# Kernel tuning notes

Hardware: AMD Instinct MI355X
Metric: run time of the kernel (lower is better)

## Reference

```python
import jax, jax.numpy as jnp
import numpy as np

ALPHA = 0.0005
TAU = 0.2


def setup_inputs() -> dict:
    key = jax.random.key(0)
    k1, k2, k3 = jax.random.split(key, 3)
    x_batch = jax.random.normal(k1, (2048, 4096), dtype=jnp.float32)
    y_batch = jax.random.normal(k2, (2048, 4096), dtype=jnp.float32)
    # conv weight [out_ch, in_ch, kh, kw]; sliced along dim 2 (F = 64)
    conv_w = jax.random.normal(k3, (512, 512, 64, 3), dtype=jnp.float32) * 0.05
    return {"x_batch": x_batch, "y_batch": y_batch, "conv_w": conv_w}


def _diversity_reg(conv_w, tau):
    # slices conv_w[:, :, i, :] flattened -> rows of v: [F, out*in*kw]
    F = conv_w.shape[2]
    v = jnp.transpose(conv_w, (2, 0, 1, 3)).reshape(F, -1)
    norms = jnp.sqrt(jnp.sum(v * v, axis=1))  # [F]
    gram = v @ v.T  # [F, F] -- memory-bound tall-skinny reduction
    sim = gram / (norms[:, None] * norms[None, :])
    eye = jnp.eye(F, dtype=bool)
    # keep iff tau < sim <= 1 and i != j; zeroed entries are detached (constant 0)
    mask = (sim > tau) & (sim <= 1.0) & (~eye)
    return jnp.sum(jnp.where(mask, sim, 0.0))


def reference(x_batch, y_batch, conv_w):
    # loss_function = MSELoss (mean reduction)
    loss_value = jnp.mean((x_batch - y_batch) ** 2)
    reg_value = _diversity_reg(conv_w, TAU)
    return loss_value + ALPHA * reg_value
```

## Files before the change

kernel.cpp:

```cpp
#include <hip/hip_runtime.h>

typedef __attribute__((ext_vector_type(8)))  short   short8;
typedef __attribute__((ext_vector_type(4)))  unsigned uint4v;
typedef __attribute__((ext_vector_type(16))) float   f32x16;
typedef __attribute__((ext_vector_type(4)))  float   f4;

constexpr int GRAM_BLOCKS = 384;
constexpr int MSE_BLOCKS  = 128;
constexpr int BLOCK       = 256;
constexpr int CHUNK_F     = 3072;
constexpr int NCHUNK      = 16384;
constexpr int GRAM_WAVES  = GRAM_BLOCKS * 4;
constexpr int MSE_THREADS = MSE_BLOCKS * BLOCK;
constexpr int RED_BLOCKS  = 96;

constexpr int MSE_OFF  = 0;
constexpr int FLAG_OFF = 128;
constexpr int GF_OFF   = 256;
constexpr int PART_OFF = 4096;

struct F3 { float v[3]; };
struct Chunk { F3 a0[4], a1[4], b0[4], b1[4]; };

__device__ __forceinline__ unsigned pk_bf16(float a, float b) {
  unsigned a2 = __builtin_bit_cast(unsigned, a) + 0x8000u;
  unsigned b2 = __builtin_bit_cast(unsigned, b) + 0x8000u;
  return __builtin_amdgcn_perm(b2, a2, 0x07060302u);
}

__device__ __forceinline__ void load_chunk(const float* __restrict__ W, int c,
                                           int laneoff, Chunk& ch) {
  const float* s = W + (size_t)c * CHUNK_F + laneoff;
#pragma unroll
  for (int bp = 0; bp < 4; ++bp) {
    const float* p = s + bp * 384;
    ch.a0[bp] = *(const F3*)(p);
    ch.a1[bp] = *(const F3*)(p + 96);
    ch.b0[bp] = *(const F3*)(p + 192);
    ch.b1[bp] = *(const F3*)(p + 288);
  }
}

__device__ __forceinline__ void mac_chunk(const Chunk& c, f32x16& a00, f32x16& a01,
                                          f32x16& a11) {
#pragma unroll
  for (int k = 0; k < 3; ++k) {
    unsigned fl[4], fh[4];
#pragma unroll
    for (int bp = 0; bp < 4; ++bp) {
      fl[bp] = pk_bf16(c.a0[bp].v[k], c.b0[bp].v[k]);
      fh[bp] = pk_bf16(c.a1[bp].v[k], c.b1[bp].v[k]);
    }
    uint4v vl = {fl[0], fl[1], fl[2], fl[3]};
    uint4v vh = {fh[0], fh[1], fh[2], fh[3]};
    short8 lo = __builtin_bit_cast(short8, vl);
    short8 hv = __builtin_bit_cast(short8, vh);
    a00 = __builtin_amdgcn_mfma_f32_32x32x16_bf16(lo, lo, a00, 0, 0, 0);
    a01 = __builtin_amdgcn_mfma_f32_32x32x16_bf16(lo, hv, a01, 0, 0, 0);
    a11 = __builtin_amdgcn_mfma_f32_32x32x16_bf16(hv, hv, a11, 0, 0, 0);
  }
}

__global__ __launch_bounds__(BLOCK, 2) void k_a(
    const float* __restrict__ X, const float* __restrict__ Y,
    const float* __restrict__ W, float* __restrict__ ws) {
  __shared__ __align__(16) float red[2][3072];
  const int bid = blockIdx.x;
  const int tid = threadIdx.x;
  const int wave = tid >> 6;
  const int lane = tid & 63;

  if (bid >= GRAM_BLOCKS) {
    const unsigned t0 = (unsigned)((bid - GRAM_BLOCKS) * BLOCK + tid);
    const f4* x4 = (const f4*)X;
    const f4* y4 = (const f4*)Y;
    float acc = 0.f;
#pragma unroll 8
    for (int it = 0; it < 64; ++it) {
      unsigned i = t0 + (unsigned)it * (unsigned)MSE_THREADS;
      f4 a = __builtin_nontemporal_load(x4 + i);
      f4 b = __builtin_nontemporal_load(y4 + i);
      float d0 = a[0] - b[0], d1 = a[1] - b[1], d2 = a[2] - b[2], d3 = a[3] - b[3];
      acc += d0 * d0 + d1 * d1 + d2 * d2 + d3 * d3;
    }
#pragma unroll
    for (int o = 32; o; o >>= 1) acc += __shfl_xor(acc, o, 64);
    __shared__ float wsum[4];
    if (lane == 0) wsum[wave] = acc;
    __syncthreads();
    if (tid == 0) ws[MSE_OFF + bid - GRAM_BLOCKS] = wsum[0] + wsum[1] + wsum[2] + wsum[3];
    return;
  }

  const int r    = lane & 31;
  const int hi   = lane >> 5;
  const int laneoff = hi * 1536 + 3 * r;
  const int wg = bid * 4 + wave;

  f32x16 a00{}, a01{}, a11{};
  Chunk ca, cb;
  int c = wg;
  load_chunk(W, c, laneoff, ca);
  c += GRAM_WAVES;
  for (;;) {
    if (c < NCHUNK) load_chunk(W, c, laneoff, cb);
    mac_chunk(ca, a00, a01, a11);
    if (c >= NCHUNK) break;
    c += GRAM_WAVES;
    if (c < NCHUNK) load_chunk(W, c, laneoff, ca);
    mac_chunk(cb, a00, a01, a11);
    if (c >= NCHUNK) break;
    c += GRAM_WAVES;
  }

  if (wave < 2) {
#pragma unroll
    for (int rg = 0; rg < 16; ++rg) {
      red[wave][       rg * 64 + lane] = a00[rg];
      red[wave][1024 + rg * 64 + lane] = a01[rg];
      red[wave][2048 + rg * 64 + lane] = a11[rg];
    }
  }
  __syncthreads();
  if (wave >= 2) {
    float* dst = red[wave - 2];
#pragma unroll
    for (int rg = 0; rg < 16; ++rg) {
      dst[       rg * 64 + lane] += a00[rg];
      dst[1024 + rg * 64 + lane] += a01[rg];
      dst[2048 + rg * 64 + lane] += a11[rg];
    }
  }
  __syncthreads();
  const f4* r0 = (const f4*)&red[0][0];
  const f4* r1 = (const f4*)&red[1][0];
  f4* p4 = (f4*)(ws + PART_OFF + (size_t)bid * 3072);
#pragma unroll
  for (int q = tid; q < 768; q += BLOCK) {
    f4 a = r0[q], b = r1[q];
    p4[q] = a + b;
  }
}

__global__ __launch_bounds__(256) void k_b(float* __restrict__ ws,
                                           float* __restrict__ out) {
  __shared__ float r2[4][32];
  __shared__ float g[3072];
  __shared__ float n2[64];
  __shared__ float msum_s[4];
  __shared__ float wsum[4];
  const int tid = threadIdx.x;
  const int lane = tid & 63, wv = tid >> 6, el = lane & 31, ph = lane >> 5;
  const int b = blockIdx.x;
  const int w0 = b * 32;
  int* flags = (int*)(ws + FLAG_OFF);

  const float* base = ws + PART_OFF + (size_t)(ph + 2 * wv) * 3072 + w0 + el;
  float acc = 0.f;
#pragma unroll 8
  for (int i = 0; i < 48; ++i) acc += base[(size_t)i * 24576];
  acc += __shfl_xor(acc, 32, 64);
  if (ph == 0) r2[wv][el] = acc;
  __syncthreads();
  if (tid < 32)
    ws[GF_OFF + w0 + tid] = r2[0][tid] + r2[1][tid] + r2[2][tid] + r2[3][tid];
  __syncthreads();
  if (tid == 0) {
    __threadfence();
    __hip_atomic_store(&flags[b], 1, __ATOMIC_RELEASE, __HIP_MEMORY_SCOPE_AGENT);
  }
  if (b != 0) return;

  if (tid < RED_BLOCKS) {
    while (__hip_atomic_load(&flags[tid], __ATOMIC_RELAXED,
                             __HIP_MEMORY_SCOPE_AGENT) != 1)
      __builtin_amdgcn_s_sleep(8);
  }
  __syncthreads();
  __threadfence();

  for (int e = tid; e < 3072; e += 256) g[e] = ws[GF_OFF + e];

  float m = (tid < 128) ? ws[MSE_OFF + tid] : 0.f;
#pragma unroll
  for (int o = 32; o; o >>= 1) m += __shfl_xor(m, o, 64);
  if (lane == 0) msum_s[wv] = m;
  __syncthreads();

  if (tid < RED_BLOCKS) flags[tid] = 0;

  for (int e = tid; e < 3072; e += 256) {
    int tl = e >> 10, rg = (e >> 6) & 15, l = e & 63;
    int il = (rg & 3) + 8 * (rg >> 2) + 4 * (l >> 5);
    int jl = l & 31;
    if (tl != 1 && il == jl) n2[il + (tl == 2 ? 32 : 0)] = g[e];
  }
  __syncthreads();

  float local = 0.f;
  for (int e = tid; e < 3072; e += 256) {
    int tl = e >> 10, rg = (e >> 6) & 15, l = e & 63;
    int il = (rg & 3) + 8 * (rg >> 2) + 4 * (l >> 5);
    int jl = l & 31;
    int i, j; float wgt;
    if (tl == 0)      { i = il;      j = jl;      wgt = 1.f; }
    else if (tl == 1) { i = il;      j = jl + 32; wgt = 2.f; }
    else              { i = il + 32; j = jl + 32; wgt = 1.f; }
    if (i != j) {
      float sim = g[e] / sqrtf(n2[i] * n2[j]);
      if (sim > 0.2f && sim <= 1.0f) local += wgt * sim;
    }
  }
#pragma unroll
  for (int o = 32; o; o >>= 1) local += __shfl_xor(local, o, 64);
  if (lane == 0) wsum[wv] = local;
  __syncthreads();
  if (tid == 0) {
    float reg_sum = wsum[0] + wsum[1] + wsum[2] + wsum[3];
    float mse_sum = msum_s[0] + msum_s[1] + msum_s[2] + msum_s[3];
    out[0] = mse_sum * (1.0f / 8388608.0f) + 0.0005f * reg_sum;
  }
}

extern "C" void kernel_launch(void* const* d_in, const int* in_sizes, int n_in,
                              void* d_out, int out_size, void* d_ws, size_t ws_size,
                              hipStream_t stream) {
  const float* X = (const float*)d_in[0];
  const float* Y = (const float*)d_in[1];
  const float* W = (const float*)d_in[2];
  float* ws = (float*)d_ws;

  k_a<<<GRAM_BLOCKS + MSE_BLOCKS, BLOCK, 0, stream>>>(X, Y, W, ws);
  k_b<<<RED_BLOCKS, 256, 0, stream>>>(ws, (float*)d_out);
}
```

Baseline: 61.63 us.

## Fuse gram, MSE and reduction into one kernel with flag-based grid sync

```diff
diff --git a/kernel.cpp b/kernel.cpp
--- a/kernel.cpp
+++ b/kernel.cpp
@@ -5,19 +5,18 @@
 typedef __attribute__((ext_vector_type(16))) float   f32x16;
 typedef __attribute__((ext_vector_type(4)))  float   f4;
 
-constexpr int GRAM_BLOCKS = 384;
-constexpr int MSE_BLOCKS  = 128;
-constexpr int BLOCK       = 256;
-constexpr int CHUNK_F     = 3072;
-constexpr int NCHUNK      = 16384;
-constexpr int GRAM_WAVES  = GRAM_BLOCKS * 4;
-constexpr int MSE_THREADS = MSE_BLOCKS * BLOCK;
-constexpr int RED_BLOCKS  = 96;
+constexpr int NBLOCK     = 512;
+constexpr int BLOCK      = 256;
+constexpr int CHUNK_F    = 3072;
+constexpr int CPW        = 8;
+constexpr int RED_BLOCKS = 96;
+constexpr int MSE_ITERS  = 16;
 
 constexpr int MSE_OFF  = 0;
-constexpr int FLAG_OFF = 128;
-constexpr int GF_OFF   = 256;
-constexpr int PART_OFF = 4096;
+constexpr int F1_OFF   = 512;
+constexpr int F2_OFF   = 1024;
+constexpr int GF_OFF   = 1152;
+constexpr int PART_OFF = 4608;
 
 struct F3 { float v[3]; };
 struct Chunk { F3 a0[4], a1[4], b0[4], b1[4]; };
@@ -61,23 +60,72 @@
   }
 }
 
-__global__ __launch_bounds__(BLOCK, 2) void k_a(
+__global__ __launch_bounds__(BLOCK, 2) void k_all(
     const float* __restrict__ X, const float* __restrict__ Y,
-    const float* __restrict__ W, float* __restrict__ ws) {
+    const float* __restrict__ W, float* __restrict__ ws,
+    float* __restrict__ out) {
   __shared__ __align__(16) float red[2][3072];
-  const int bid = blockIdx.x;
-  const int tid = threadIdx.x;
+  __shared__ float r2[4][32];
+  __shared__ float n2[64];
+  __shared__ float fsum[4];
+  const int bid  = blockIdx.x;
+  const int tid  = threadIdx.x;
   const int wave = tid >> 6;
   const int lane = tid & 63;
-
-  if (bid >= GRAM_BLOCKS) {
-    const unsigned t0 = (unsigned)((bid - GRAM_BLOCKS) * BLOCK + tid);
+  const int r    = lane & 31;
+  const int hi   = lane >> 5;
+  int* flag1 = (int*)(ws + F1_OFF);
+  int* flag2 = (int*)(ws + F2_OFF);
+
+  const int laneoff = hi * 1536 + 3 * r;
+  const int c0 = bid * 32 + wave * 8;
+
+  f32x16 a00{}, a01{}, a11{};
+  Chunk ca, cb;
+  load_chunk(W, c0, laneoff, ca);
+#pragma unroll
+  for (int t = 0; t < CPW; t += 2) {
+    load_chunk(W, c0 + t + 1, laneoff, cb);
+    mac_chunk(ca, a00, a01, a11);
+    if (t + 2 < CPW) load_chunk(W, c0 + t + 2, laneoff, ca);
+    mac_chunk(cb, a00, a01, a11);
+  }
+
+  if (wave < 2) {
+#pragma unroll
+    for (int rg = 0; rg < 16; ++rg) {
+      red[wave][       rg * 64 + lane] = a00[rg];
+      red[wave][1024 + rg * 64 + lane] = a01[rg];
+      red[wave][2048 + rg * 64 + lane] = a11[rg];
+    }
+  }
+  __syncthreads();
+  if (wave >= 2) {
+    float* dst = red[wave - 2];
+#pragma unroll
+    for (int rg = 0; rg < 16; ++rg) {
+      dst[       rg * 64 + lane] += a00[rg];
+      dst[1024 + rg * 64 + lane] += a01[rg];
+      dst[2048 + rg * 64 + lane] += a11[rg];
+    }
+  }
+  __syncthreads();
+  {
+    const f4* r0 = (const f4*)&red[0][0];
+    const f4* r1 = (const f4*)&red[1][0];
+    f4* p4 = (f4*)(ws + PART_OFF + (size_t)bid * 3072);
+#pragma unroll
+    for (int q = tid; q < 768; q += BLOCK) p4[q] = r0[q] + r1[q];
+  }
+
+  {
     const f4* x4 = (const f4*)X;
     const f4* y4 = (const f4*)Y;
     float acc = 0.f;
 #pragma unroll 8
-    for (int it = 0; it < 64; ++it) {
-      unsigned i = t0 + (unsigned)it * (unsigned)MSE_THREADS;
+    for (int j = 0; j < MSE_ITERS; ++j) {
+      unsigned i = (unsigned)j * (unsigned)(NBLOCK * BLOCK) +
+                   (unsigned)bid * BLOCK + (unsigned)tid;
       f4 a = __builtin_nontemporal_load(x4 + i);
       f4 b = __builtin_nontemporal_load(y4 + i);
       float d0 = a[0] - b[0], d1 = a[1] - b[1], d2 = a[2] - b[2], d3 = a[3] - b[3];
@@ -85,111 +133,65 @@
     }
 #pragma unroll
     for (int o = 32; o; o >>= 1) acc += __shfl_xor(acc, o, 64);
-    __shared__ float wsum[4];
-    if (lane == 0) wsum[wave] = acc;
+    if (lane == 0) fsum[wave] = acc;
     __syncthreads();
-    if (tid == 0) ws[MSE_OFF + bid - GRAM_BLOCKS] = wsum[0] + wsum[1] + wsum[2] + wsum[3];
-    return;
-  }
-
-  const int r    = lane & 31;
-  const int hi   = lane >> 5;
-  const int laneoff = hi * 1536 + 3 * r;
-  const int wg = bid * 4 + wave;
-
-  f32x16 a00{}, a01{}, a11{};
-  Chunk ca, cb;
-  int c = wg;
-  load_chunk(W, c, laneoff, ca);
-  c += GRAM_WAVES;
-  for (;;) {
-    if (c < NCHUNK) load_chunk(W, c, laneoff, cb);
-    mac_chunk(ca, a00, a01, a11);
-    if (c >= NCHUNK) break;
-    c += GRAM_WAVES;
-    if (c < NCHUNK) load_chunk(W, c, laneoff, ca);
-    mac_chunk(cb, a00, a01, a11);
-    if (c >= NCHUNK) break;
-    c += GRAM_WAVES;
-  }
-
-  if (wave < 2) {
-#pragma unroll
-    for (int rg = 0; rg < 16; ++rg) {
-      red[wave][       rg * 64 + lane] = a00[rg];
-      red[wave][1024 + rg * 64 + lane] = a01[rg];
-      red[wave][2048 + rg * 64 + lane] = a11[rg];
-    }
-  }
-  __syncthreads();
-  if (wave >= 2) {
-    float* dst = red[wave - 2];
-#pragma unroll
-    for (int rg = 0; rg < 16; ++rg) {
-      dst[       rg * 64 + lane] += a00[rg];
-      dst[1024 + rg * 64 + lane] += a01[rg];
-      dst[2048 + rg * 64 + lane] += a11[rg];
-    }
-  }
-  __syncthreads();
-  const f4* r0 = (const f4*)&red[0][0];
-  const f4* r1 = (const f4*)&red[1][0];
-  f4* p4 = (f4*)(ws + PART_OFF + (size_t)bid * 3072);
-#pragma unroll
-  for (int q = tid; q < 768; q += BLOCK) {
-    f4 a = r0[q], b = r1[q];
-    p4[q] = a + b;
-  }
-}
-
-__global__ __launch_bounds__(256) void k_b(float* __restrict__ ws,
-                                           float* __restrict__ out) {
-  __shared__ float r2[4][32];
-  __shared__ float g[3072];
-  __shared__ float n2[64];
-  __shared__ float msum_s[4];
-  __shared__ float wsum[4];
-  const int tid = threadIdx.x;
-  const int lane = tid & 63, wv = tid >> 6, el = lane & 31, ph = lane >> 5;
-  const int b = blockIdx.x;
-  const int w0 = b * 32;
-  int* flags = (int*)(ws + FLAG_OFF);
-
-  const float* base = ws + PART_OFF + (size_t)(ph + 2 * wv) * 3072 + w0 + el;
-  float acc = 0.f;
-#pragma unroll 8
-  for (int i = 0; i < 48; ++i) acc += base[(size_t)i * 24576];
-  acc += __shfl_xor(acc, 32, 64);
-  if (ph == 0) r2[wv][el] = acc;
-  __syncthreads();
-  if (tid < 32)
-    ws[GF_OFF + w0 + tid] = r2[0][tid] + r2[1][tid] + r2[2][tid] + r2[3][tid];
+    if (tid == 0) ws[MSE_OFF + bid] = fsum[0] + fsum[1] + fsum[2] + fsum[3];
+  }
+
   __syncthreads();
   if (tid == 0) {
     __threadfence();
-    __hip_atomic_store(&flags[b], 1, __ATOMIC_RELEASE, __HIP_MEMORY_SCOPE_AGENT);
-  }
-  if (b != 0) return;
-
-  if (tid < RED_BLOCKS) {
-    while (__hip_atomic_load(&flags[tid], __ATOMIC_RELAXED,
+    __hip_atomic_store(&flag1[bid], 1, __ATOMIC_RELEASE, __HIP_MEMORY_SCOPE_AGENT);
+  }
+
+  if (bid >= RED_BLOCKS) return;
+  for (int f = tid; f < NBLOCK; f += BLOCK)
+    while (__hip_atomic_load(&flag1[f], __ATOMIC_RELAXED,
                              __HIP_MEMORY_SCOPE_AGENT) != 1)
-      __builtin_amdgcn_s_sleep(8);
-  }
+      __builtin_amdgcn_s_sleep(4);
   __syncthreads();
   __threadfence();
 
-  for (int e = tid; e < 3072; e += 256) g[e] = ws[GF_OFF + e];
-
-  float m = (tid < 128) ? ws[MSE_OFF + tid] : 0.f;
+  {
+    const int el = lane & 31, ph = lane >> 5;
+    const int w0 = bid * 32;
+    const float* base = ws + PART_OFF + (size_t)(ph + 2 * wave) * 3072 + w0 + el;
+    float acc = 0.f;
+#pragma unroll 8
+    for (int i = 0; i < 64; ++i) acc += base[(size_t)i * 24576];
+    acc += __shfl_xor(acc, 32, 64);
+    if (ph == 0) r2[wave][el] = acc;
+    __syncthreads();
+    if (tid < 32)
+      ws[GF_OFF + w0 + tid] = r2[0][tid] + r2[1][tid] + r2[2][tid] + r2[3][tid];
+  }
+  __syncthreads();
+  if (tid == 0) {
+    __threadfence();
+    __hip_atomic_store(&flag2[bid], 1, __ATOMIC_RELEASE, __HIP_MEMORY_SCOPE_AGENT);
+  }
+
+  if (bid != 0) return;
+  if (tid < RED_BLOCKS)
+    while (__hip_atomic_load(&flag2[tid], __ATOMIC_RELAXED,
+                             __HIP_MEMORY_SCOPE_AGENT) != 1)
+      __builtin_amdgcn_s_sleep(4);
+  __syncthreads();
+  __threadfence();
+
+  float* g = &red[0][0];
+  for (int e = tid; e < 3072; e += BLOCK) g[e] = ws[GF_OFF + e];
+
+  float m = ws[MSE_OFF + tid] + ws[MSE_OFF + 256 + tid];
 #pragma unroll
   for (int o = 32; o; o >>= 1) m += __shfl_xor(m, o, 64);
-  if (lane == 0) msum_s[wv] = m;
-  __syncthreads();
-
-  if (tid < RED_BLOCKS) flags[tid] = 0;
-
-  for (int e = tid; e < 3072; e += 256) {
+  if (lane == 0) fsum[wave] = m;
+
+  for (int f = tid; f < NBLOCK; f += BLOCK) flag1[f] = 0;
+  if (tid < RED_BLOCKS) flag2[tid] = 0;
+  __syncthreads();
+
+  for (int e = tid; e < 3072; e += BLOCK) {
     int tl = e >> 10, rg = (e >> 6) & 15, l = e & 63;
     int il = (rg & 3) + 8 * (rg >> 2) + 4 * (l >> 5);
     int jl = l & 31;
@@ -198,7 +200,7 @@
   __syncthreads();
 
   float local = 0.f;
-  for (int e = tid; e < 3072; e += 256) {
+  for (int e = tid; e < 3072; e += BLOCK) {
     int tl = e >> 10, rg = (e >> 6) & 15, l = e & 63;
     int il = (rg & 3) + 8 * (rg >> 2) + 4 * (l >> 5);
     int jl = l & 31;
@@ -213,11 +215,12 @@
   }
 #pragma unroll
   for (int o = 32; o; o >>= 1) local += __shfl_xor(local, o, 64);
-  if (lane == 0) wsum[wv] = local;
+  __shared__ float wsum[4];
+  if (lane == 0) wsum[wave] = local;
   __syncthreads();
   if (tid == 0) {
     float reg_sum = wsum[0] + wsum[1] + wsum[2] + wsum[3];
-    float mse_sum = msum_s[0] + msum_s[1] + msum_s[2] + msum_s[3];
+    float mse_sum = fsum[0] + fsum[1] + fsum[2] + fsum[3];
     out[0] = mse_sum * (1.0f / 8388608.0f) + 0.0005f * reg_sum;
   }
 }
@@ -228,8 +231,5 @@
   const float* X = (const float*)d_in[0];
   const float* Y = (const float*)d_in[1];
   const float* W = (const float*)d_in[2];
-  float* ws = (float*)d_ws;
-
-  k_a<<<GRAM_BLOCKS + MSE_BLOCKS, BLOCK, 0, stream>>>(X, Y, W, ws);
-  k_b<<<RED_BLOCKS, 256, 0, stream>>>(ws, (float*)d_out);
-}
+  k_all<<<NBLOCK, BLOCK, 0, stream>>>(X, Y, W, (float*)d_ws, (float*)d_out);
+}
```

After: 104.5 us. +69.5%, slower.

## Fuse MSE into every gram wave with 1024-thread blocks and fixed chunk counts

Applied to the files above, without the earlier changes.

```diff
diff --git a/kernel.cpp b/kernel.cpp
--- a/kernel.cpp
+++ b/kernel.cpp
@@ -5,18 +5,15 @@
 typedef __attribute__((ext_vector_type(16))) float   f32x16;
 typedef __attribute__((ext_vector_type(4)))  float   f4;
 
-constexpr int GRAM_BLOCKS = 384;
-constexpr int MSE_BLOCKS  = 128;
-constexpr int BLOCK       = 256;
-constexpr int CHUNK_F     = 3072;
-constexpr int NCHUNK      = 16384;
-constexpr int GRAM_WAVES  = GRAM_BLOCKS * 4;
-constexpr int MSE_THREADS = MSE_BLOCKS * BLOCK;
-constexpr int RED_BLOCKS  = 96;
+constexpr int NB         = 256;
+constexpr int BLOCK      = 1024;
+constexpr int CHUNK_F    = 3072;
+constexpr int CPW        = 4;
+constexpr int RED_BLOCKS = 96;
 
 constexpr int MSE_OFF  = 0;
-constexpr int FLAG_OFF = 128;
-constexpr int GF_OFF   = 256;
+constexpr int FLAG_OFF = 256;
+constexpr int GF_OFF   = 512;
 constexpr int PART_OFF = 4096;
 
 struct F3 { float v[3]; };
@@ -61,84 +58,86 @@
   }
 }
 
-__global__ __launch_bounds__(BLOCK, 2) void k_a(
+__device__ __forceinline__ float mse2(const f4* x4, const f4* y4, int i0) {
+  f4 xa = __builtin_nontemporal_load(x4 + i0 * 64);
+  f4 ya = __builtin_nontemporal_load(y4 + i0 * 64);
+  f4 xb = __builtin_nontemporal_load(x4 + (i0 + 1) * 64);
+  f4 yb = __builtin_nontemporal_load(y4 + (i0 + 1) * 64);
+  f4 d0 = xa - ya, d1 = xb - yb;
+  return d0[0]*d0[0] + d0[1]*d0[1] + d0[2]*d0[2] + d0[3]*d0[3] +
+         d1[0]*d1[0] + d1[1]*d1[1] + d1[2]*d1[2] + d1[3]*d1[3];
+}
+
+__global__ __launch_bounds__(BLOCK, 4) void k_a(
     const float* __restrict__ X, const float* __restrict__ Y,
     const float* __restrict__ W, float* __restrict__ ws) {
-  __shared__ __align__(16) float red[2][3072];
-  const int bid = blockIdx.x;
-  const int tid = threadIdx.x;
+  __shared__ __align__(16) float red[4][3072];
+  __shared__ float fsum[16];
+  const int bid  = blockIdx.x;
+  const int tid  = threadIdx.x;
   const int wave = tid >> 6;
   const int lane = tid & 63;
-
-  if (bid >= GRAM_BLOCKS) {
-    const unsigned t0 = (unsigned)((bid - GRAM_BLOCKS) * BLOCK + tid);
-    const f4* x4 = (const f4*)X;
-    const f4* y4 = (const f4*)Y;
-    float acc = 0.f;
-#pragma unroll 8
-    for (int it = 0; it < 64; ++it) {
-      unsigned i = t0 + (unsigned)it * (unsigned)MSE_THREADS;
-      f4 a = __builtin_nontemporal_load(x4 + i);
-      f4 b = __builtin_nontemporal_load(y4 + i);
-      float d0 = a[0] - b[0], d1 = a[1] - b[1], d2 = a[2] - b[2], d3 = a[3] - b[3];
-      acc += d0 * d0 + d1 * d1 + d2 * d2 + d3 * d3;
-    }
-#pragma unroll
-    for (int o = 32; o; o >>= 1) acc += __shfl_xor(acc, o, 64);
-    __shared__ float wsum[4];
-    if (lane == 0) wsum[wave] = acc;
-    __syncthreads();
-    if (tid == 0) ws[MSE_OFF + bid - GRAM_BLOCKS] = wsum[0] + wsum[1] + wsum[2] + wsum[3];
-    return;
-  }
-
   const int r    = lane & 31;
   const int hi   = lane >> 5;
+  const int wid  = bid * 16 + wave;
   const int laneoff = hi * 1536 + 3 * r;
-  const int wg = bid * 4 + wave;
+  const int c0 = wid * CPW;
+  const f4* x4 = (const f4*)X + (size_t)wid * 512 + lane;
+  const f4* y4 = (const f4*)Y + (size_t)wid * 512 + lane;
 
   f32x16 a00{}, a01{}, a11{};
+  float macc = 0.f;
   Chunk ca, cb;
-  int c = wg;
-  load_chunk(W, c, laneoff, ca);
-  c += GRAM_WAVES;
-  for (;;) {
-    if (c < NCHUNK) load_chunk(W, c, laneoff, cb);
+  load_chunk(W, c0, laneoff, ca);
+#pragma unroll
+  for (int t = 0; t < CPW; t += 2) {
+    load_chunk(W, c0 + t + 1, laneoff, cb);
+    macc += mse2(x4, y4, 2 * t);
     mac_chunk(ca, a00, a01, a11);
-    if (c >= NCHUNK) break;
-    c += GRAM_WAVES;
-    if (c < NCHUNK) load_chunk(W, c, laneoff, ca);
+    if (t + 2 < CPW) load_chunk(W, c0 + t + 2, laneoff, ca);
+    macc += mse2(x4, y4, 2 * t + 2);
     mac_chunk(cb, a00, a01, a11);
-    if (c >= NCHUNK) break;
-    c += GRAM_WAVES;
-  }
-
-  if (wave < 2) {
-#pragma unroll
-    for (int rg = 0; rg < 16; ++rg) {
-      red[wave][       rg * 64 + lane] = a00[rg];
-      red[wave][1024 + rg * 64 + lane] = a01[rg];
-      red[wave][2048 + rg * 64 + lane] = a11[rg];
+  }
+
+#pragma unroll
+  for (int o = 32; o; o >>= 1) macc += __shfl_xor(macc, o, 64);
+  if (lane == 0) fsum[wave] = macc;
+
+#pragma unroll
+  for (int rd = 0; rd < 4; ++rd) {
+    if ((wave >> 2) == rd) {
+      float* dst = red[wave & 3];
+      if (rd == 0) {
+#pragma unroll
+        for (int rg = 0; rg < 16; ++rg) {
+          dst[       rg * 64 + lane] = a00[rg];
+          dst[1024 + rg * 64 + lane] = a01[rg];
+          dst[2048 + rg * 64 + lane] = a11[rg];
+        }
+      } else {
+#pragma unroll
+        for (int rg = 0; rg < 16; ++rg) {
+          dst[       rg * 64 + lane] += a00[rg];
+          dst[1024 + rg * 64 + lane] += a01[rg];
+          dst[2048 + rg * 64 + lane] += a11[rg];
+        }
+      }
     }
-  }
-  __syncthreads();
-  if (wave >= 2) {
-    float* dst = red[wave - 2];
-#pragma unroll
-    for (int rg = 0; rg < 16; ++rg) {
-      dst[       rg * 64 + lane] += a00[rg];
-      dst[1024 + rg * 64 + lane] += a01[rg];
-      dst[2048 + rg * 64 + lane] += a11[rg];
-    }
-  }
-  __syncthreads();
-  const f4* r0 = (const f4*)&red[0][0];
-  const f4* r1 = (const f4*)&red[1][0];
-  f4* p4 = (f4*)(ws + PART_OFF + (size_t)bid * 3072);
-#pragma unroll
-  for (int q = tid; q < 768; q += BLOCK) {
-    f4 a = r0[q], b = r1[q];
-    p4[q] = a + b;
+    __syncthreads();
+  }
+  {
+    const f4* r0 = (const f4*)&red[0][0];
+    const f4* r1 = (const f4*)&red[1][0];
+    const f4* r2 = (const f4*)&red[2][0];
+    const f4* r3 = (const f4*)&red[3][0];
+    f4* p4 = (f4*)(ws + PART_OFF + (size_t)bid * 3072);
+    if (tid < 768) p4[tid] = r0[tid] + r1[tid] + r2[tid] + r3[tid];
+  }
+  if (tid == 0) {
+    float m = 0.f;
+#pragma unroll
+    for (int wv = 0; wv < 16; ++wv) m += fsum[wv];
+    ws[MSE_OFF + bid] = m;
   }
 }
 
@@ -158,7 +157,7 @@
   const float* base = ws + PART_OFF + (size_t)(ph + 2 * wv) * 3072 + w0 + el;
   float acc = 0.f;
 #pragma unroll 8
-  for (int i = 0; i < 48; ++i) acc += base[(size_t)i * 24576];
+  for (int i = 0; i < 32; ++i) acc += base[(size_t)i * 24576];
   acc += __shfl_xor(acc, 32, 64);
   if (ph == 0) r2[wv][el] = acc;
   __syncthreads();
@@ -171,17 +170,16 @@
   }
   if (b != 0) return;
 
-  if (tid < RED_BLOCKS) {
+  if (tid < RED_BLOCKS)
     while (__hip_atomic_load(&flags[tid], __ATOMIC_RELAXED,
                              __HIP_MEMORY_SCOPE_AGENT) != 1)
       __builtin_amdgcn_s_sleep(8);
-  }
   __syncthreads();
   __threadfence();
 
   for (int e = tid; e < 3072; e += 256) g[e] = ws[GF_OFF + e];
 
-  float m = (tid < 128) ? ws[MSE_OFF + tid] : 0.f;
+  float m = ws[MSE_OFF + tid];
 #pragma unroll
   for (int o = 32; o; o >>= 1) m += __shfl_xor(m, o, 64);
   if (lane == 0) msum_s[wv] = m;
@@ -228,8 +226,6 @@
   const float* X = (const float*)d_in[0];
   const float* Y = (const float*)d_in[1];
   const float* W = (const float*)d_in[2];
-  float* ws = (float*)d_ws;
-
-  k_a<<<GRAM_BLOCKS + MSE_BLOCKS, BLOCK, 0, stream>>>(X, Y, W, ws);
-  k_b<<<RED_BLOCKS, 256, 0, stream>>>(ws, (float*)d_out);
-}
+  k_a<<<NB, BLOCK, 0, stream>>>(X, Y, W, (float*)d_ws);
+  k_b<<<RED_BLOCKS, 256, 0, stream>>>((float*)d_ws, (float*)d_out);
+}
```

After: 76.30 us. 23.8% more time.
